# Kernel tuning notes

Hardware: AMD Instinct MI355X
Metric: run time of the kernel (lower is better)

The kernel has to match this reference:

```python
import jax, jax.numpy as jnp
import numpy as np

NUM_HEADS = 2
ROPE_BASE = 10000.0


def _rope_tables(seq_len, head_dim, dtype):
    # inv_freq over even indices of head_dim
    inv_freq = 1.0 / (ROPE_BASE ** (jnp.arange(0, head_dim, 2, dtype=jnp.float32) / head_dim))
    t = jnp.arange(seq_len, dtype=jnp.float32)
    freqs = t[:, None] * inv_freq[None, :]            # (s, head_dim/2)
    emb = jnp.concatenate([freqs, freqs], axis=-1)    # (s, head_dim)
    return jnp.cos(emb).astype(dtype), jnp.sin(emb).astype(dtype)


def _apply_rotation(x_bsd, cos, sin):
    # x_bsd: (b, s, h*d); chunk in half along last dim (h=2 -> halves == head_dim)
    x1, x2 = jnp.split(x_bsd, 2, axis=-1)
    return jnp.concatenate([x1 * cos - x2 * sin, x2 * cos + x1 * sin], axis=-1)


def setup_inputs() -> dict:
    key = jax.random.key(0)
    k1, k2, k3, k4 = jax.random.split(key, 4)
    b, s, dim = 4, 2048, 2048
    x = jax.random.normal(k1, (b, s, dim), dtype=jnp.float32)
    wqkv = jax.random.normal(k2, (dim, 3 * dim), dtype=jnp.float32) * (dim ** -0.5)
    wout = jax.random.normal(k3, (dim, dim), dtype=jnp.float32) * (dim ** -0.5)
    bout = jax.random.normal(k4, (dim,), dtype=jnp.float32) * 0.01
    return {"x": x, "wqkv": wqkv, "wout": wout, "bout": bout}


def reference(x, wqkv, wout, bout):
    b, s, dim = x.shape
    h = NUM_HEADS
    d = dim // h
    scale = d ** -0.5

    qkv = x @ wqkv                                    # (b, s, 3*dim)
    qkv = qkv.reshape(b, s, 3, h, d).transpose(2, 0, 3, 1, 4)  # (3, b, h, s, d)
    q, k, v = qkv[0], qkv[1], qkv[2]                  # (b, h, s, d)

    # RoPE applied on (b, s, h*d) layout, exactly as source
    cos, sin = _rope_tables(s, d, x.dtype)            # (s, d) each
    q_flat = q.transpose(0, 2, 1, 3).reshape(b, s, h * d)
    k_flat = k.transpose(0, 2, 1, 3).reshape(b, s, h * d)
    q = _apply_rotation(q_flat, cos, sin).reshape(b, s, h, d).transpose(0, 2, 1, 3)
    k = _apply_rotation(k_flat, cos, sin).reshape(b, s, h, d).transpose(0, 2, 1, 3)

    scores = jnp.einsum('bhid,bhjd->bhij', q, k) * scale
    attn = jax.nn.softmax(scores, axis=-1)
    out = jnp.einsum('bhij,bhjd->bhid', attn, v)      # (b, h, s, d)
    out = out.transpose(0, 2, 1, 3).reshape(b, s, dim)
    return out @ wout + bout
```

## Files before the change

### kernel.cpp

```cpp
#include <hip/hip_runtime.h>
#include <hip/hip_fp16.h>

typedef __attribute__((ext_vector_type(4))) float f32x4;
typedef __attribute__((ext_vector_type(16))) float f32x16;
typedef __attribute__((ext_vector_type(8))) _Float16 f16x8;
typedef __attribute__((ext_vector_type(4))) _Float16 f16x4;

__device__ __forceinline__ void gload_lds16(const void* gp, void* lp) {
    __builtin_amdgcn_global_load_lds(
        (const __attribute__((address_space(1))) void*)gp,
        (__attribute__((address_space(3))) void*)lp, 16, 0, 0);
}

__device__ __forceinline__ void barrier_fenced() {
    asm volatile("s_barrier" ::: "memory");
}

__global__ void rope_tables_k(float* __restrict__ cosT, float* __restrict__ sinT) {
    int idx = blockIdx.x * 256 + threadIdx.x;
    int s = idx >> 9, j = idx & 511;
    float invf = exp2f(-13.287712379549449f * (float)j * (1.0f / 512.0f));
    float ang = (float)s * invf;
    float sn, cs;
    sincosf(ang, &sn, &cs);
    cosT[idx] = cs;
    sinT[idx] = sn;
}

__global__ void f32_to_f16_vec(const float* __restrict__ in, _Float16* __restrict__ out) {
    long i = ((long)blockIdx.x * 256 + threadIdx.x) * 4;
    f32x4 v = *(const f32x4*)(in + i);
    f16x4 h;
#pragma unroll
    for (int e = 0; e < 4; ++e) h[e] = (_Float16)v[e];
    *(f16x4*)(out + i) = h;
}

__global__ void transpose_f32_to_f16(const float* __restrict__ in, _Float16* __restrict__ out,
                                     int R, int C) {
    __shared__ _Float16 tile[32][36];
    const int c0 = blockIdx.x * 32, r0 = blockIdx.y * 32;
    const int t = threadIdx.x;
    const int r = t >> 3, c4 = (t & 7) * 4;
    f32x4 v = *(const f32x4*)(in + (long)(r0 + r) * C + c0 + c4);
    f16x4 h;
#pragma unroll
    for (int e = 0; e < 4; ++e) h[e] = (_Float16)v[e];
    *(f16x4*)&tile[r][c4] = h;
    __syncthreads();
    const int oc = t >> 3, o4 = (t & 7) * 4;
    f16x4 o;
#pragma unroll
    for (int e = 0; e < 4; ++e) o[e] = tile[o4 + e][oc];
    *(f16x4*)(out + (long)(c0 + oc) * R + r0 + o4) = o;
}

__global__ void rope_inplace(_Float16* __restrict__ qkv, const float* __restrict__ cosT,
                             const float* __restrict__ sinT) {
    const int row = blockIdx.x;
    const int s = row & 2047;
    const int j0 = threadIdx.x * 4;
    _Float16* base = qkv + (long)row * 6144;
    f16x4 q0 = *(const f16x4*)(base + j0);
    f16x4 q1 = *(const f16x4*)(base + 1024 + j0);
    f16x4 k0 = *(const f16x4*)(base + 2048 + j0);
    f16x4 k1 = *(const f16x4*)(base + 3072 + j0);
    const int jj = j0 & 511;
    f32x4 cs = *(const f32x4*)(cosT + (long)s * 512 + jj);
    f32x4 sn = *(const f32x4*)(sinT + (long)s * 512 + jj);
    f16x4 oq0, oq1, ok0, ok1;
#pragma unroll
    for (int e = 0; e < 4; ++e) {
        float a = (float)q0[e], b = (float)q1[e];
        oq0[e] = (_Float16)(a * cs[e] - b * sn[e]);
        oq1[e] = (_Float16)(b * cs[e] + a * sn[e]);
        float c = (float)k0[e], d = (float)k1[e];
        ok0[e] = (_Float16)(c * cs[e] - d * sn[e]);
        ok1[e] = (_Float16)(d * cs[e] + c * sn[e]);
    }
    *(f16x4*)(base + j0) = oq0;
    *(f16x4*)(base + 1024 + j0) = oq1;
    *(f16x4*)(base + 2048 + j0) = ok0;
    *(f16x4*)(base + 3072 + j0) = ok1;
}

__global__ void v_transpose(const _Float16* __restrict__ qkv, _Float16* __restrict__ vT) {
    __shared__ _Float16 tile[32][36];
    const int z = blockIdx.z, b = z >> 1, h = z & 1;
    const int s0 = blockIdx.x * 32, d0 = blockIdx.y * 32;
    const int t = threadIdx.x;
    const int r = t >> 3, c4 = (t & 7) * 4;
    const _Float16* src = qkv + (long)(b * 2048 + s0 + r) * 6144 + 4096 + h * 1024 + d0 + c4;
    *(f16x4*)&tile[r][c4] = *(const f16x4*)src;
    __syncthreads();
    const int dr = t >> 3, sc = (t & 7) * 4;
    f16x4 o;
#pragma unroll
    for (int e = 0; e < 4; ++e) o[e] = tile[sc + e][dr];
    *(f16x4*)(vT + ((long)z * 1024 + d0 + dr) * 2048 + s0 + sc) = o;
}

__global__ __launch_bounds__(256) void softmax_rows_f32(float* __restrict__ S, float scale) {
    const int wid = threadIdx.x >> 6, lane = threadIdx.x & 63;
    const long row = (long)blockIdx.x * 4 + wid;
    float* rp = S + row * 2048;
    f32x4 v[8];
    float mx = -1e30f;
#pragma unroll
    for (int i = 0; i < 8; ++i) {
        v[i] = *(const f32x4*)(rp + (i * 64 + lane) * 4);
#pragma unroll
        for (int e = 0; e < 4; ++e) mx = fmaxf(mx, v[i][e]);
    }
#pragma unroll
    for (int o = 32; o > 0; o >>= 1) mx = fmaxf(mx, __shfl_xor(mx, o, 64));
    float sum = 0.f;
#pragma unroll
    for (int i = 0; i < 8; ++i)
#pragma unroll
        for (int e = 0; e < 4; ++e) {
            float p = __expf(scale * (v[i][e] - mx));
            v[i][e] = p; sum += p;
        }
#pragma unroll
    for (int o = 32; o > 0; o >>= 1) sum += __shfl_xor(sum, o, 64);
    float inv = 1.0f / sum;
    _Float16* wp = (_Float16*)S + row * 4096;
#pragma unroll
    for (int i = 0; i < 8; ++i) {
        f16x4 h;
#pragma unroll
        for (int e = 0; e < 4; ++e) h[e] = (_Float16)(v[i][e] * inv);
        *(f16x4*)(wp + (i * 64 + lane) * 4) = h;
    }
}

__global__ __launch_bounds__(256) void rowsum_f16(const _Float16* __restrict__ S,
                                                  float* __restrict__ l) {
    const int wid = threadIdx.x >> 6, lane = threadIdx.x & 63;
    const long row = (long)blockIdx.x * 4 + wid;
    const _Float16* rp = S + row * 2048;
    float sum = 0.f;
#pragma unroll
    for (int i = 0; i < 4; ++i) {
        f16x8 v = *(const f16x8*)(rp + i * 512 + lane * 8);
#pragma unroll
        for (int e = 0; e < 8; ++e) sum += (float)v[e];
    }
#pragma unroll
    for (int o = 32; o > 0; o >>= 1) sum += __shfl_xor(sum, o, 64);
    if (lane == 0) l[row] = sum;
}

template <int OMODE, bool BIAS>
__global__ __launch_bounds__(256, 2)
void gemm32(const _Float16* __restrict__ A, const _Float16* __restrict__ B,
            void* __restrict__ Cv, const float* __restrict__ aux, float scale,
            int K, int lda, int ldb, int ldc, int zmod,
            long a1, long a2, long b1, long b2, long c1, long c2) {
    __shared__ char lds[73728];
    const int z = blockIdx.z, zq = z / zmod, zr = z - zq * zmod;
    A += zq * a1 + zr * a2;
    B += zq * b1 + zr * b2;
    const long coff = zq * c1 + zr * c2;
    const int tm = blockIdx.y * 256, tn = blockIdx.x * 128;
    const int t = threadIdx.x;
    const int lane = t & 63, wid = t >> 6;
    const int wr = wid >> 1, wc = wid & 1;
    const int l31 = lane & 31, kg = lane >> 5;

    const int strow = t >> 2;
    const int stcol = 8 * ((t & 3) ^ ((t >> 3) & 3));
    const _Float16* gA = A + (long)(tm + strow) * lda + stcol;
    const _Float16* gB = B + (long)(tn + strow) * ldb + stcol;
    const int ldsw = wid * 1024;

    const int rsw = (l31 >> 1) & 3;
    const int sw0 = 16 * ((0 + kg) ^ rsw);
    const int sw1 = 16 * ((2 + kg) ^ rsw);
    const int abase = (wr * 128 + l31) * 64;
    const int bbase = 16384 + (wc * 64 + l31) * 64;

    const int NT = K >> 5;
    f32x16 acc[4][2] = {};

    auto stage = [&](int tt, int slot) {
        const long ko = (long)tt * 32;
        char* d = lds + slot * 24576 + ldsw;
#pragma unroll
        for (int i = 0; i < 4; ++i)
            gload_lds16(gA + ko + (long)(i * 64) * lda, d + i * 4096);
#pragma unroll
        for (int i = 0; i < 2; ++i)
            gload_lds16(gB + ko + (long)(i * 64) * ldb, d + 16384 + i * 4096);
    };

    stage(0, 0);
    stage(1, 1);

    int st = 0, sp = 2;
    for (int tt = 0; tt < NT; ++tt) {
        if (tt + 1 < NT) asm volatile("s_waitcnt vmcnt(6)" ::: "memory");
        else             asm volatile("s_waitcnt vmcnt(0)" ::: "memory");
        barrier_fenced();
        const char* buf = lds + st * 24576;
        f16x8 af[4][2], bf[2][2];
#pragma unroll
        for (int m = 0; m < 4; ++m) {
            af[m][0] = *(const f16x8*)(buf + abase + m * 2048 + sw0);
            af[m][1] = *(const f16x8*)(buf + abase + m * 2048 + sw1);
        }
#pragma unroll
        for (int n = 0; n < 2; ++n) {
            bf[n][0] = *(const f16x8*)(buf + bbase + n * 2048 + sw0);
            bf[n][1] = *(const f16x8*)(buf + bbase + n * 2048 + sw1);
        }
        if (tt + 2 < NT) stage(tt + 2, sp);
        __builtin_amdgcn_s_setprio(1);
#pragma unroll
        for (int ks = 0; ks < 2; ++ks)
#pragma unroll
            for (int m = 0; m < 4; ++m)
#pragma unroll
                for (int n = 0; n < 2; ++n)
                    acc[m][n] = __builtin_amdgcn_mfma_f32_32x32x16_f16(af[m][ks], bf[n][ks], acc[m][n], 0, 0, 0);
        __builtin_amdgcn_s_setprio(0);
        st = (st == 2) ? 0 : st + 1;
        sp = (sp == 2) ? 0 : sp + 1;
    }

    const int rb = tm + wr * 128;
    const int cb = tn + wc * 64 + l31;
    const float* auxz = (OMODE == 3) ? (aux + (long)z * 2048) : aux;
#pragma unroll
    for (int m = 0; m < 4; ++m) {
#pragma unroll
        for (int r = 0; r < 16; ++r) {
            const int rloc = (r & 3) + 8 * (r >> 2) + 4 * kg;
            const int row = rb + m * 32 + rloc;
            float inv = 1.0f;
            if (OMODE == 3) inv = __builtin_amdgcn_rcpf(auxz[row]);
#pragma unroll
            for (int n = 0; n < 2; ++n) {
                float v = acc[m][n][r];
                const int col = cb + n * 32;
                if (BIAS) v += aux[col];
                if (OMODE == 0) {
                    ((float*)Cv)[coff + (long)row * ldc + col] = v;
                } else {
                    if (OMODE == 2) v = __expf(v * scale);
                    if (OMODE == 3) v *= inv;
                    ((_Float16*)Cv)[coff + (long)row * ldc + col] = (_Float16)v;
                }
            }
        }
    }
}

extern "C" void kernel_launch(void* const* d_in, const int* in_sizes, int n_in,
                              void* d_out, int out_size, void* d_ws, size_t ws_size,
                              hipStream_t stream) {
    const float* x    = (const float*)d_in[0];
    const float* wqkv = (const float*)d_in[1];
    const float* wout = (const float*)d_in[2];
    const float* bout = (const float*)d_in[3];
    char* ws = (char*)d_ws;

    _Float16* qkv_h = (_Float16*)(ws);
    _Float16* x_h   = (_Float16*)(ws + 100663296);
    _Float16* wqkvT = (_Float16*)(ws + 134217728);
    _Float16* vT    = (_Float16*)(ws + 100663296);
    float*    cosT  = (float*)(ws + 100663296);
    float*    sinT  = (float*)(ws + 104857600);
    _Float16* woutT = (_Float16*)(ws);
    const bool batched = ws_size >= 234946560ULL;

    f32_to_f16_vec<<<dim3(16384), dim3(256), 0, stream>>>(x, x_h);
    transpose_f32_to_f16<<<dim3(192, 64), dim3(256), 0, stream>>>(wqkv, wqkvT, 2048, 6144);
    gemm32<1, false><<<dim3(48, 32, 1), dim3(256), 0, stream>>>(
        x_h, wqkvT, (void*)qkv_h, nullptr, 0.f, 2048, 2048, 2048, 6144,
        1, 0L, 0L, 0L, 0L, 0L, 0L);
    rope_tables_k<<<dim3(4096), dim3(256), 0, stream>>>(cosT, sinT);
    rope_inplace<<<dim3(8192), dim3(256), 0, stream>>>(qkv_h, cosT, sinT);
    v_transpose<<<dim3(64, 32, 8), dim3(256), 0, stream>>>(qkv_h, vT);

    if (batched) {
        _Float16* S16  = (_Float16*)(ws + 134217728);
        _Float16* aout = (_Float16*)(ws + 201326592);
        float*    lsum = (float*)(ws + 234881024);
        gemm32<2, false><<<dim3(16, 8, 8), dim3(256), 0, stream>>>(
            qkv_h, qkv_h + 2048, (void*)S16, nullptr, 0.03125f, 1024, 6144, 6144, 2048,
            2, 12582912L, 1024L, 12582912L, 1024L, 8388608L, 4194304L);
        rowsum_f16<<<dim3(4096), dim3(256), 0, stream>>>(S16, lsum);
        gemm32<3, false><<<dim3(8, 8, 8), dim3(256), 0, stream>>>(
            S16, vT, (void*)aout, lsum, 0.f, 2048, 2048, 2048, 2048,
            2, 8388608L, 4194304L, 4194304L, 2097152L, 4194304L, 1024L);
        transpose_f32_to_f16<<<dim3(64, 64), dim3(256), 0, stream>>>(wout, woutT, 2048, 2048);
        gemm32<0, true><<<dim3(16, 32, 1), dim3(256), 0, stream>>>(
            aout, woutT, d_out, bout, 0.f, 2048, 2048, 2048, 2048,
            1, 0L, 0L, 0L, 0L, 0L, 0L);
    } else {
        float*    S32  = (float*)(ws + 134217728);
        _Float16* aout = (_Float16*)(ws + 150994944);
        for (int z = 0; z < 8; ++z) {
            const _Float16* Az = qkv_h + (long)(z >> 1) * 12582912 + (z & 1) * 1024;
            gemm32<0, false><<<dim3(16, 8, 1), dim3(256), 0, stream>>>(
                Az, Az + 2048, (void*)S32, nullptr, 0.f, 1024, 6144, 6144, 2048,
                1, 0L, 0L, 0L, 0L, 0L, 0L);
            softmax_rows_f32<<<dim3(512), dim3(256), 0, stream>>>(S32, 0.03125f);
            gemm32<1, false><<<dim3(8, 8, 1), dim3(256), 0, stream>>>(
                (const _Float16*)S32, vT + (long)z * 2097152,
                (void*)(aout + (long)(z >> 1) * 4194304 + (z & 1) * 1024), nullptr, 0.f,
                2048, 4096, 2048, 2048, 1, 0L, 0L, 0L, 0L, 0L, 0L);
        }
        transpose_f32_to_f16<<<dim3(64, 64), dim3(256), 0, stream>>>(wout, woutT, 2048, 2048);
        gemm32<0, true><<<dim3(16, 32, 1), dim3(256), 0, stream>>>(
            aout, woutT, d_out, bout, 0.f, 2048, 2048, 2048, 2048,
            1, 0L, 0L, 0L, 0L, 0L, 0L);
    }
}
```

Before: 581.3 us.

## Rework GEMM to 16x16x32 MFMA with B fragments loaded directly to registers

The shared GEMM kernel switches from 32x32x16 to 16x16x32 MFMA tiles. Only the A tile is staged through LDS, which shrinks LDS from 72KB to 48KB. B fragments now come straight from global memory into double-buffered registers, and the main loop is unrolled by two with a rotating three-slot A buffer. The aim is to cut LDS traffic and footprint and overlap B loads with compute. The cost is more uncoalesced global loads for B and more accumulator registers (8x4 f32x4), which may strain occupancy at launch_bounds(256,2).

```diff
diff --git a/kernel.cpp b/kernel.cpp
--- a/kernel.cpp
+++ b/kernel.cpp
@@ -2,7 +2,6 @@
 #include <hip/hip_fp16.h>
 
 typedef __attribute__((ext_vector_type(4))) float f32x4;
-typedef __attribute__((ext_vector_type(16))) float f32x16;
 typedef __attribute__((ext_vector_type(8))) _Float16 f16x8;
 typedef __attribute__((ext_vector_type(4))) _Float16 f16x4;
 
@@ -154,11 +153,11 @@
 
 template <int OMODE, bool BIAS>
 __global__ __launch_bounds__(256, 2)
-void gemm32(const _Float16* __restrict__ A, const _Float16* __restrict__ B,
-            void* __restrict__ Cv, const float* __restrict__ aux, float scale,
-            int K, int lda, int ldb, int ldc, int zmod,
-            long a1, long a2, long b1, long b2, long c1, long c2) {
-    __shared__ char lds[73728];
+void gemmh(const _Float16* __restrict__ A, const _Float16* __restrict__ B,
+           void* __restrict__ Cv, const float* __restrict__ aux, float scale,
+           int K, int lda, int ldb, int ldc, int zmod,
+           long a1, long a2, long b1, long b2, long c1, long c2) {
+    __shared__ char lds[49152];
     const int z = blockIdx.z, zq = z / zmod, zr = z - zq * zmod;
     A += zq * a1 + zr * a2;
     B += zq * b1 + zr * b2;
@@ -167,83 +166,95 @@
     const int t = threadIdx.x;
     const int lane = t & 63, wid = t >> 6;
     const int wr = wid >> 1, wc = wid & 1;
-    const int l31 = lane & 31, kg = lane >> 5;
+    const int fr = lane & 15, kg = lane >> 4;
 
     const int strow = t >> 2;
     const int stcol = 8 * ((t & 3) ^ ((t >> 3) & 3));
     const _Float16* gA = A + (long)(tm + strow) * lda + stcol;
-    const _Float16* gB = B + (long)(tn + strow) * ldb + stcol;
     const int ldsw = wid * 1024;
 
-    const int rsw = (l31 >> 1) & 3;
-    const int sw0 = 16 * ((0 + kg) ^ rsw);
-    const int sw1 = 16 * ((2 + kg) ^ rsw);
-    const int abase = (wr * 128 + l31) * 64;
-    const int bbase = 16384 + (wc * 64 + l31) * 64;
+    const int swz = 16 * (kg ^ ((fr >> 1) & 3));
+    const int abase = (wr * 128 + fr) * 64 + swz;
+
+    const _Float16* gBf = B + (long)(tn + wc * 64 + fr) * ldb + kg * 8;
+    const long bstep = (long)16 * ldb;
 
     const int NT = K >> 5;
-    f32x16 acc[4][2] = {};
-
-    auto stage = [&](int tt, int slot) {
-        const long ko = (long)tt * 32;
-        char* d = lds + slot * 24576 + ldsw;
+    f32x4 acc[8][4] = {};
+    f16x8 bfA[4], bfB[4];
+
+    auto stageA = [&](int tt, int slot) {
+        const _Float16* s = gA + (long)tt * 32;
+        char* d = lds + slot * 16384 + ldsw;
 #pragma unroll
         for (int i = 0; i < 4; ++i)
-            gload_lds16(gA + ko + (long)(i * 64) * lda, d + i * 4096);
-#pragma unroll
-        for (int i = 0; i < 2; ++i)
-            gload_lds16(gB + ko + (long)(i * 64) * ldb, d + 16384 + i * 4096);
+            gload_lds16(s + (long)(i * 64) * lda, d + i * 4096);
     };
-
-    stage(0, 0);
-    stage(1, 1);
-
-    int st = 0, sp = 2;
-    for (int tt = 0; tt < NT; ++tt) {
-        if (tt + 1 < NT) asm volatile("s_waitcnt vmcnt(6)" ::: "memory");
-        else             asm volatile("s_waitcnt vmcnt(0)" ::: "memory");
+#define LOADB(tt, bf) do { const _Float16* sb_ = gBf + (long)(tt) * 32; \
+        bf[0] = *(const f16x8*)(sb_);             bf[1] = *(const f16x8*)(sb_ + bstep); \
+        bf[2] = *(const f16x8*)(sb_ + 2 * bstep); bf[3] = *(const f16x8*)(sb_ + 3 * bstep); } while (0)
+
+    stageA(0, 0);
+    LOADB(0, bfA);
+    stageA(1, 1);
+    LOADB(1, bfB);
+
+    int sa = 0, sb = 1, sc = 2;
+    for (int i = 0; i < NT; i += 2) {
+        asm volatile("s_waitcnt vmcnt(8)" ::: "memory");
         barrier_fenced();
-        const char* buf = lds + st * 24576;
-        f16x8 af[4][2], bf[2][2];
-#pragma unroll
-        for (int m = 0; m < 4; ++m) {
-            af[m][0] = *(const f16x8*)(buf + abase + m * 2048 + sw0);
-            af[m][1] = *(const f16x8*)(buf + abase + m * 2048 + sw1);
-        }
-#pragma unroll
-        for (int n = 0; n < 2; ++n) {
-            bf[n][0] = *(const f16x8*)(buf + bbase + n * 2048 + sw0);
-            bf[n][1] = *(const f16x8*)(buf + bbase + n * 2048 + sw1);
-        }
-        if (tt + 2 < NT) stage(tt + 2, sp);
-        __builtin_amdgcn_s_setprio(1);
-#pragma unroll
-        for (int ks = 0; ks < 2; ++ks)
-#pragma unroll
-            for (int m = 0; m < 4; ++m)
-#pragma unroll
-                for (int n = 0; n < 2; ++n)
-                    acc[m][n] = __builtin_amdgcn_mfma_f32_32x32x16_f16(af[m][ks], bf[n][ks], acc[m][n], 0, 0, 0);
-        __builtin_amdgcn_s_setprio(0);
-        st = (st == 2) ? 0 : st + 1;
-        sp = (sp == 2) ? 0 : sp + 1;
-    }
-
-    const int rb = tm + wr * 128;
-    const int cb = tn + wc * 64 + l31;
+        {
+            const char* buf = lds + sa * 16384;
+            f16x8 af[8];
+#pragma unroll
+            for (int m = 0; m < 8; ++m) af[m] = *(const f16x8*)(buf + abase + m * 1024);
+            if (i + 2 < NT) stageA(i + 2, sc);
+            __builtin_amdgcn_s_setprio(1);
+#pragma unroll
+            for (int m = 0; m < 8; ++m)
+#pragma unroll
+                for (int n = 0; n < 4; ++n)
+                    acc[m][n] = __builtin_amdgcn_mfma_f32_16x16x32_f16(af[m], bfA[n], acc[m][n], 0, 0, 0);
+            __builtin_amdgcn_s_setprio(0);
+            if (i + 2 < NT) LOADB(i + 2, bfA);
+        }
+        if (i + 2 < NT) asm volatile("s_waitcnt vmcnt(8)" ::: "memory");
+        else            asm volatile("s_waitcnt vmcnt(0)" ::: "memory");
+        barrier_fenced();
+        {
+            const char* buf = lds + sb * 16384;
+            f16x8 af[8];
+#pragma unroll
+            for (int m = 0; m < 8; ++m) af[m] = *(const f16x8*)(buf + abase + m * 1024);
+            if (i + 3 < NT) stageA(i + 3, sa);
+            __builtin_amdgcn_s_setprio(1);
+#pragma unroll
+            for (int m = 0; m < 8; ++m)
+#pragma unroll
+                for (int n = 0; n < 4; ++n)
+                    acc[m][n] = __builtin_amdgcn_mfma_f32_16x16x32_f16(af[m], bfB[n], acc[m][n], 0, 0, 0);
+            __builtin_amdgcn_s_setprio(0);
+            if (i + 3 < NT) LOADB(i + 3, bfB);
+        }
+        const int na = sc, nb = sa, nc = sb;
+        sa = na; sb = nb; sc = nc;
+    }
+#undef LOADB
+
+    const int rb = tm + wr * 128 + (lane >> 4) * 4;
+    const int cb = tn + wc * 64 + fr;
     const float* auxz = (OMODE == 3) ? (aux + (long)z * 2048) : aux;
 #pragma unroll
-    for (int m = 0; m < 4; ++m) {
-#pragma unroll
-        for (int r = 0; r < 16; ++r) {
-            const int rloc = (r & 3) + 8 * (r >> 2) + 4 * kg;
-            const int row = rb + m * 32 + rloc;
+    for (int m = 0; m < 8; ++m) {
+#pragma unroll
+        for (int r = 0; r < 4; ++r) {
+            const int row = rb + m * 16 + r;
             float inv = 1.0f;
             if (OMODE == 3) inv = __builtin_amdgcn_rcpf(auxz[row]);
 #pragma unroll
-            for (int n = 0; n < 2; ++n) {
+            for (int n = 0; n < 4; ++n) {
                 float v = acc[m][n][r];
-                const int col = cb + n * 32;
+                const int col = cb + n * 16;
                 if (BIAS) v += aux[col];
                 if (OMODE == 0) {
                     ((float*)Cv)[coff + (long)row * ldc + col] = v;
@@ -277,7 +288,7 @@
 
     f32_to_f16_vec<<<dim3(16384), dim3(256), 0, stream>>>(x, x_h);
     transpose_f32_to_f16<<<dim3(192, 64), dim3(256), 0, stream>>>(wqkv, wqkvT, 2048, 6144);
-    gemm32<1, false><<<dim3(48, 32, 1), dim3(256), 0, stream>>>(
+    gemmh<1, false><<<dim3(48, 32, 1), dim3(256), 0, stream>>>(
         x_h, wqkvT, (void*)qkv_h, nullptr, 0.f, 2048, 2048, 2048, 6144,
         1, 0L, 0L, 0L, 0L, 0L, 0L);
     rope_tables_k<<<dim3(4096), dim3(256), 0, stream>>>(cosT, sinT);
@@ -288,15 +299,15 @@
         _Float16* S16  = (_Float16*)(ws + 134217728);
         _Float16* aout = (_Float16*)(ws + 201326592);
         float*    lsum = (float*)(ws + 234881024);
-        gemm32<2, false><<<dim3(16, 8, 8), dim3(256), 0, stream>>>(
+        gemmh<2, false><<<dim3(16, 8, 8), dim3(256), 0, stream>>>(
             qkv_h, qkv_h + 2048, (void*)S16, nullptr, 0.03125f, 1024, 6144, 6144, 2048,
             2, 12582912L, 1024L, 12582912L, 1024L, 8388608L, 4194304L);
         rowsum_f16<<<dim3(4096), dim3(256), 0, stream>>>(S16, lsum);
-        gemm32<3, false><<<dim3(8, 8, 8), dim3(256), 0, stream>>>(
+        gemmh<3, false><<<dim3(8, 8, 8), dim3(256), 0, stream>>>(
             S16, vT, (void*)aout, lsum, 0.f, 2048, 2048, 2048, 2048,
             2, 8388608L, 4194304L, 4194304L, 2097152L, 4194304L, 1024L);
         transpose_f32_to_f16<<<dim3(64, 64), dim3(256), 0, stream>>>(wout, woutT, 2048, 2048);
-        gemm32<0, true><<<dim3(16, 32, 1), dim3(256), 0, stream>>>(
+        gemmh<0, true><<<dim3(16, 32, 1), dim3(256), 0, stream>>>(
             aout, woutT, d_out, bout, 0.f, 2048, 2048, 2048, 2048,
             1, 0L, 0L, 0L, 0L, 0L, 0L);
     } else {
@@ -304,17 +315,17 @@
         _Float16* aout = (_Float16*)(ws + 150994944);
         for (int z = 0; z < 8; ++z) {
             const _Float16* Az = qkv_h + (long)(z >> 1) * 12582912 + (z & 1) * 1024;
-            gemm32<0, false><<<dim3(16, 8, 1), dim3(256), 0, stream>>>(
+            gemmh<0, false><<<dim3(16, 8, 1), dim3(256), 0, stream>>>(
                 Az, Az + 2048, (void*)S32, nullptr, 0.f, 1024, 6144, 6144, 2048,
                 1, 0L, 0L, 0L, 0L, 0L, 0L);
             softmax_rows_f32<<<dim3(512), dim3(256), 0, stream>>>(S32, 0.03125f);
-            gemm32<1, false><<<dim3(8, 8, 1), dim3(256), 0, stream>>>(
+            gemmh<1, false><<<dim3(8, 8, 1), dim3(256), 0, stream>>>(
                 (const _Float16*)S32, vT + (long)z * 2097152,
                 (void*)(aout + (long)(z >> 1) * 4194304 + (z & 1) * 1024), nullptr, 0.f,
                 2048, 4096, 2048, 2048, 1, 0L, 0L, 0L, 0L, 0L, 0L);
         }
         transpose_f32_to_f16<<<dim3(64, 64), dim3(256), 0, stream>>>(wout, woutT, 2048, 2048);
-        gemm32<0, true><<<dim3(16, 32, 1), dim3(256), 0, stream>>>(
+        gemmh<0, true><<<dim3(16, 32, 1), dim3(256), 0, stream>>>(
             aout, woutT, d_out, bout, 0.f, 2048, 2048, 2048, 2048,
             1, 0L, 0L, 0L, 0L, 0L, 0L);
     }
```

Result: slower. 667.7 us (+14.9%).
